# Kernel tuning notes

Hardware: AMD Instinct MI355X
Metric: run time of the kernel (lower is better)

The kernel has to match this reference:

```python
import jax, jax.numpy as jnp
import numpy as np


def setup_inputs() -> dict:
    key = jax.random.key(0)
    ks = jax.random.split(key, 9)
    B, C, H, W = 16, 512, 56, 56
    I = C // 2
    return {
        "x": jax.random.normal(ks[0], (B, C, H, W), dtype=jnp.float32),
        "g_w": jax.random.normal(ks[1], (I, C), dtype=jnp.float32) * 0.02,
        "g_b": jax.random.normal(ks[2], (I,), dtype=jnp.float32) * 0.02,
        "theta_w": jax.random.normal(ks[3], (I, C), dtype=jnp.float32) * 0.02,
        "theta_b": jax.random.normal(ks[4], (I,), dtype=jnp.float32) * 0.02,
        "phi_w": jax.random.normal(ks[5], (I, C), dtype=jnp.float32) * 0.02,
        "phi_b": jax.random.normal(ks[6], (I,), dtype=jnp.float32) * 0.02,
        "W_w": jax.random.normal(ks[7], (C, I), dtype=jnp.float32) * 0.02,
        "W_b": jax.random.normal(ks[8], (C,), dtype=jnp.float32) * 0.02,
    }


def reference(x, g_w, g_b, theta_w, theta_b, phi_w, phi_b, W_w, W_b):
    B, C, H, W = x.shape
    N = H * W
    xf = x.reshape(B, C, N)  # flatten spatial -> [B, C, N]
    # 1x1 convs == per-pixel channel matmuls
    g = jnp.einsum('ic,bcn->bin', g_w, xf) + g_b[:, None]        # [B, I, N]
    th = jnp.einsum('ic,bcn->bin', theta_w, xf) + theta_b[:, None]
    ph = jnp.einsum('ic,bcn->bin', phi_w, xf) + phi_b[:, None]
    # Original: y = (theta^T @ phi / N) @ g^T. No softmax -> reassociate:
    # y = theta^T @ ((phi @ g^T) / N), avoiding the [B, N, N] score matrix.
    M = jnp.einsum('bjn,bin->bji', ph, g) / N                    # [B, I, I]
    y = jnp.einsum('bjn,bji->bin', th, M)                        # [B, I, N]
    out = jnp.einsum('ci,bin->bcn', W_w, y) + W_b[:, None]       # [B, C, N]
    return x + out.reshape(B, C, H, W)
```

## Files before the change

kernel.cpp:

```cpp
#include <hip/hip_runtime.h>
#include <stdint.h>


typedef unsigned short ushort_t;
typedef __attribute__((ext_vector_type(8))) short short8;
typedef __attribute__((ext_vector_type(4))) float f32x4;
typedef __attribute__((ext_vector_type(8))) unsigned short us8;

#define NSP  3136

#define AS1(p) ((const __attribute__((address_space(1))) void*)(p))
#define AS3(p) ((__attribute__((address_space(3))) void*)(p))

__device__ inline ushort_t f2b(float f) {
  union { float f; uint32_t u; } c; c.f = f;
  uint32_t u = c.u;
  uint32_t r = (u + 0x7fffu + ((u >> 16) & 1u)) >> 16;
  return (ushort_t)r;
}

template<int MODE>
__global__ __launch_bounds__(256, 2) void gemm64(
    const ushort_t* __restrict__ Abase,
    const ushort_t* __restrict__ Bbase,
    void* __restrict__ Cbase, void* __restrict__ C2,
    const float* __restrict__ bias,
    const float* __restrict__ xres)
{
  constexpr int TB = 256;
  constexpr int CH = TB / 8;

  const int nwg = gridDim.x * gridDim.y * gridDim.z;
  int flat = blockIdx.x + gridDim.x * (blockIdx.y + gridDim.y * blockIdx.z);
  const int q = nwg >> 3;
  int swz = (flat & 7) * q + (flat >> 3);
  const int bx = swz % gridDim.x; int tmp = swz / gridDim.x;
  const int by = tmp % gridDim.y;
  const int bz = tmp / gridDim.y;

  int b = bz, kc = 0, kbeg = 0, kend, lda, ldb;
  const ushort_t *A, *B;
  if constexpr (MODE == 1) {
    A = Abase;
    B = Bbase + (size_t)b * 1605632;
    lda = 512; ldb = 512; kend = 512;
  } else if constexpr (MODE == 2) {
    b = bz & 15; kc = bz >> 4;
    A = Abase + (size_t)b * 1605632 + 802816;
    B = Abase + (size_t)b * 1605632;
    lda = NSP; ldb = NSP; kbeg = kc * 448; kend = kbeg + 448;
  } else if constexpr (MODE == 6) {
    A = Abase; lda = 256;
    B = Bbase + (size_t)b * 65536; ldb = 256;
    kend = 256;
  } else {
    A = Abase + (size_t)b * 131072; lda = 256;
    B = Bbase + (size_t)b * 819200; ldb = 256;
    kend = 256;
  }

  const int m0 = bx * 128;
  const int n0 = by * 128;
  const int tid = threadIdx.x;
  const int lane = tid & 63;
  const int wid = tid >> 6;
  const int wm = wid >> 1, wn = wid & 1;
  const int fr = lane & 15;
  const int fk = lane >> 4;

  __shared__ __align__(16) ushort_t SMu[32768];
  ushort_t (*As)[8192] = (ushort_t(*)[8192])(SMu);
  ushort_t (*Bs)[8192] = (ushort_t(*)[8192])(SMu + 16384);

  f32x4 acc[4][4];
#pragma unroll
  for (int i = 0; i < 4; ++i)
#pragma unroll
    for (int j = 0; j < 4; ++j) acc[i][j] = f32x4{0.f, 0.f, 0.f, 0.f};

  const int srow = tid >> 3;
  const int lsl = (tid & 7) ^ (srow & 7);
  const ushort_t* pa = A + (size_t)(m0 + srow) * lda + kbeg + lsl * 8;
  const ushort_t* pb = B + (size_t)(n0 + srow) * ldb + kbeg + lsl * 8;

#define STAGE(bufi) do {                                                              \
    __builtin_amdgcn_global_load_lds(AS1(pa),                    AS3(&As[bufi][tid * 8]), 16, 0, 0); \
    __builtin_amdgcn_global_load_lds(AS1(pa + (size_t)CH * lda), AS3(&As[bufi][TB * 8 + tid * 8]), 16, 0, 0); \
    __builtin_amdgcn_global_load_lds(AS1(pa + (size_t)2 * CH * lda), AS3(&As[bufi][2 * TB * 8 + tid * 8]), 16, 0, 0); \
    __builtin_amdgcn_global_load_lds(AS1(pa + (size_t)3 * CH * lda), AS3(&As[bufi][3 * TB * 8 + tid * 8]), 16, 0, 0); \
    __builtin_amdgcn_global_load_lds(AS1(pb),                    AS3(&Bs[bufi][tid * 8]), 16, 0, 0); \
    __builtin_amdgcn_global_load_lds(AS1(pb + (size_t)CH * ldb), AS3(&Bs[bufi][TB * 8 + tid * 8]), 16, 0, 0); \
    __builtin_amdgcn_global_load_lds(AS1(pb + (size_t)2 * CH * ldb), AS3(&Bs[bufi][2 * TB * 8 + tid * 8]), 16, 0, 0); \
    __builtin_amdgcn_global_load_lds(AS1(pb + (size_t)3 * CH * ldb), AS3(&Bs[bufi][3 * TB * 8 + tid * 8]), 16, 0, 0); \
    pa += 64; pb += 64;                                                               \
  } while (0)

  const int sw = fr & 7;
  const int s0 = ((0 | fk) ^ sw) * 8;
  const int s1 = ((4 | fk) ^ sw) * 8;
  const int arow = (wm * 64 + fr) * 64;
  const int brow = (wn * 64 + fr) * 64;

  asm volatile("s_waitcnt vmcnt(0)" ::: "memory");
  STAGE(0);

  const int nkt = (kend - kbeg) >> 6;
  for (int t = 0; t < nkt; ++t) {
    const int cur = t & 1;
    if (t + 1 < nkt) {
      STAGE(cur ^ 1);
      asm volatile("s_waitcnt vmcnt(8)" ::: "memory");
    } else {
      asm volatile("s_waitcnt vmcnt(0)" ::: "memory");
    }
    __builtin_amdgcn_s_barrier();
    __builtin_amdgcn_sched_barrier(0);

    short8 bf[4][2];
#pragma unroll
    for (int n = 0; n < 4; ++n) {
      bf[n][0] = *reinterpret_cast<const short8*>(&Bs[cur][brow + n * 1024 + s0]);
      bf[n][1] = *reinterpret_cast<const short8*>(&Bs[cur][brow + n * 1024 + s1]);
    }
    short8 af[4][2];
#pragma unroll
    for (int m = 0; m < 4; ++m) {
      af[m][0] = *reinterpret_cast<const short8*>(&As[cur][arow + m * 1024 + s0]);
      af[m][1] = *reinterpret_cast<const short8*>(&As[cur][arow + m * 1024 + s1]);
    }
    __builtin_amdgcn_s_setprio(1);
#pragma unroll
    for (int m = 0; m < 4; ++m)
#pragma unroll
      for (int n = 0; n < 4; ++n) {
        acc[m][n] = __builtin_amdgcn_mfma_f32_16x16x32_bf16(af[m][0], bf[n][0], acc[m][n], 0, 0, 0);
        acc[m][n] = __builtin_amdgcn_mfma_f32_16x16x32_bf16(af[m][1], bf[n][1], acc[m][n], 0, 0, 0);
      }
    __builtin_amdgcn_s_setprio(0);
    __builtin_amdgcn_s_barrier();
  }
#undef STAGE

  if constexpr (MODE == 1) {
    ushort_t* SMe = SMu;
    if (m0 < 512) {
#pragma unroll
      for (int m = 0; m < 4; ++m)
#pragma unroll
        for (int n = 0; n < 4; ++n) {
          int col = wn * 64 + n * 16 + fr;
#pragma unroll
          for (int r = 0; r < 4; ++r) {
            int row = wm * 64 + m * 16 + fk * 4 + r;
            SMe[row * 132 + col] = f2b(acc[m][n][r] + bias[m0 + row]);
          }
        }
      __builtin_amdgcn_s_barrier();
      ushort_t* P = (ushort_t*)Cbase;
#pragma unroll
      for (int it = 0; it < 8; ++it) {
        int idx = it * 256 + tid;
        int row = idx >> 4, ch = idx & 15;
        int gcol = n0 + ch * 8;
        if (gcol < NSP)
          *reinterpret_cast<us8*>(
              &P[(size_t)b * 512 * NSP + (size_t)(m0 + row) * NSP + gcol]) =
              *reinterpret_cast<const us8*>(&SMe[row * 132 + ch * 8]);
      }
    } else {
      const int j0 = m0 - 512;
#pragma unroll
      for (int m = 0; m < 4; ++m)
#pragma unroll
        for (int n = 0; n < 4; ++n) {
          int nl = wn * 64 + n * 16 + fr;
#pragma unroll
          for (int r = 0; r < 4; ++r) {
            int jl = wm * 64 + m * 16 + fk * 4 + r;
            SMe[nl * 132 + jl] = f2b(acc[m][n][r] + bias[512 + j0 + jl]);
          }
        }
      __builtin_amdgcn_s_barrier();
      ushort_t* thT = (ushort_t*)C2;
#pragma unroll
      for (int it = 0; it < 8; ++it) {
        int idx = it * 256 + tid;
        int row = idx >> 4, ch = idx & 15;
        int gn = n0 + row;
        if (gn < NSP)
          *reinterpret_cast<us8*>(
              &thT[(size_t)b * 819200 + (size_t)gn * 256 + j0 + ch * 8]) =
              *reinterpret_cast<const us8*>(&SMe[row * 132 + ch * 8]);
      }
    }
  } else if constexpr (MODE == 2) {
    float* Mf = (float*)Cbase;
#pragma unroll
    for (int m = 0; m < 4; ++m)
#pragma unroll
      for (int n = 0; n < 4; ++n) {
        int gcol = n0 + wn * 64 + n * 16 + fr;
#pragma unroll
        for (int r = 0; r < 4; ++r) {
          int grow = m0 + wm * 64 + m * 16 + fk * 4 + r;
          Mf[((size_t)kc * 16 + b) * 65536 + grow * 256 + gcol] = acc[m][n][r];
        }
      }
  } else if constexpr (MODE == 6) {
    ushort_t* U = (ushort_t*)Cbase;
#pragma unroll
    for (int m = 0; m < 4; ++m)
#pragma unroll
      for (int n = 0; n < 4; ++n) {
        int gcol = n0 + wn * 64 + n * 16 + fr;
#pragma unroll
        for (int r = 0; r < 4; ++r) {
          int grow = m0 + wm * 64 + m * 16 + fk * 4 + r;
          U[(size_t)b * 131072 + grow * 256 + gcol] = f2b(acc[m][n][r]);
        }
      }
  } else {
    float* out = (float*)Cbase;
    float* SMf = (float*)SMu;
#pragma unroll
    for (int p = 0; p < 2; ++p) {
      if (wm == p) {
#pragma unroll
        for (int m = 0; m < 4; ++m)
#pragma unroll
          for (int n = 0; n < 4; ++n) {
            int col = wn * 64 + n * 16 + fr;
#pragma unroll
            for (int r = 0; r < 4; ++r)
              SMf[(m * 16 + fk * 4 + r) * 132 + col] = acc[m][n][r];
          }
      }
      __builtin_amdgcn_s_barrier();
#pragma unroll
      for (int it = 0; it < 8; ++it) {
        int idx = it * 256 + tid;
        int row = idx >> 5, ch = idx & 31;
        int gcol = n0 + ch * 4;
        if (gcol < NSP) {
          int grow = m0 + p * 64 + row;
          size_t o = ((size_t)b * 512 + grow) * NSP + gcol;
          f32x4 v = *reinterpret_cast<const f32x4*>(&SMf[row * 132 + ch * 4]);
          f32x4 xr = *reinterpret_cast<const f32x4*>(&xres[o]);
          float bi = bias[grow];
          f32x4 ov = {v[0] + bi + xr[0], v[1] + bi + xr[1],
                      v[2] + bi + xr[2], v[3] + bi + xr[3]};
          *reinterpret_cast<f32x4*>(&out[o]) = ov;
        }
      }
      __builtin_amdgcn_s_barrier();
    }
  }
}

__global__ __launch_bounds__(256) void transp_x(const float* __restrict__ x,
                                                ushort_t* __restrict__ xb)
{
  const int nt = blockIdx.x, ct = blockIdx.y, b = blockIdx.z;
  const int t = threadIdx.x;
  const int n0 = nt * 64, c0 = ct * 64;
  __shared__ float Ls[64 * 65];

  const float* xs = x + (size_t)b * 512 * NSP;
#pragma unroll
  for (int p = 0; p < 4; ++p) {
    int cl = p * 16 + (t >> 4);
    int nl = (t & 15) * 4;
    f32x4 v = *reinterpret_cast<const f32x4*>(&xs[(size_t)(c0 + cl) * NSP + n0 + nl]);
    Ls[cl * 65 + nl + 0] = v[0];
    Ls[cl * 65 + nl + 1] = v[1];
    Ls[cl * 65 + nl + 2] = v[2];
    Ls[cl * 65 + nl + 3] = v[3];
  }
  __syncthreads();
#pragma unroll
  for (int it = 0; it < 2; ++it) {
    int idx = it * 256 + t; int nl = idx >> 3, cc = idx & 7;
    us8 o;
#pragma unroll
    for (int j = 0; j < 8; ++j) o[j] = f2b(Ls[(cc * 8 + j) * 65 + nl]);
    *reinterpret_cast<us8*>(&xb[((size_t)b * NSP + n0 + nl) * 512 + c0 + cc * 8]) = o;
  }
}

__global__ __launch_bounds__(256) void prep_weights(
    const float* __restrict__ g_w, const float* __restrict__ ph_w,
    const float* __restrict__ th_w, const float* __restrict__ W_w,
    const float* __restrict__ g_b, const float* __restrict__ ph_b,
    const float* __restrict__ th_b,
    ushort_t* __restrict__ W3, ushort_t* __restrict__ Wwb,
    float* __restrict__ bias3)
{
  int i = blockIdx.x * 256 + threadIdx.x;
  if (i < 393216) {
    int row = i >> 9, col = i & 511;
    float v = (row < 256) ? g_w[row * 512 + col]
            : (row < 512) ? ph_w[(row - 256) * 512 + col]
                          : th_w[(row - 512) * 512 + col];
    W3[i] = f2b(v);
  } else if (i < 524288) {
    Wwb[i - 393216] = f2b(W_w[i - 393216]);
  } else if (i < 525056) {
    int r = i - 524288;
    bias3[r] = (r < 256) ? g_b[r] : (r < 512) ? ph_b[r - 256] : th_b[r - 512];
  }
}

__global__ __launch_bounds__(256) void cvt_M(const float* __restrict__ Mf,
                                             ushort_t* __restrict__ MT)
{
  int i = blockIdx.x * 256 + threadIdx.x;
  const int SL = 1048576;
  float s = 0.f;
#pragma unroll
  for (int k = 0; k < 7; ++k) s += Mf[(size_t)k * SL + i];
  MT[i] = f2b(s * (1.0f / 3136.0f));
}

extern "C" void kernel_launch(void* const* d_in, const int* in_sizes, int n_in,
                              void* d_out, int out_size, void* d_ws, size_t ws_size,
                              hipStream_t stream) {
  const float* x    = (const float*)d_in[0];
  const float* g_w  = (const float*)d_in[1];
  const float* g_b  = (const float*)d_in[2];
  const float* th_w = (const float*)d_in[3];
  const float* th_b = (const float*)d_in[4];
  const float* ph_w = (const float*)d_in[5];
  const float* ph_b = (const float*)d_in[6];
  const float* W_w  = (const float*)d_in[7];
  const float* W_b  = (const float*)d_in[8];

  char* ws = (char*)d_ws;
  ushort_t* xb   = (ushort_t*)(ws + 0);
  float*    Mf2  = (float*)(ws + 0);
  ushort_t* MT2  = (ushort_t*)(ws + 29360128);
  ushort_t* U    = (ushort_t*)(ws + 31457280);
  ushort_t* P    = (ushort_t*)(ws + 51380224);
  ushort_t* thT  = (ushort_t*)(ws + 102760448);
  ushort_t* W3   = (ushort_t*)(ws + 128974848);
  ushort_t* Wwb  = (ushort_t*)(ws + 129761280);
  float*    bias3 = (float*)(ws + 130023424);

  prep_weights<<<2052, 256, 0, stream>>>(g_w, ph_w, th_w, W_w, g_b, ph_b, th_b,
                                         W3, Wwb, bias3);
  transp_x<<<dim3(49, 8, 16), 256, 0, stream>>>(x, xb);

  gemm64<1><<<dim3(6, 26, 16), 256, 0, stream>>>(W3, xb, P, thT, bias3, nullptr);
  gemm64<2><<<dim3(2, 2, 112), 256, 0, stream>>>(P, nullptr, Mf2, nullptr, nullptr, nullptr);
  cvt_M<<<4096, 256, 0, stream>>>(Mf2, MT2);
  gemm64<6><<<dim3(4, 2, 16), 256, 0, stream>>>(Wwb, MT2, U, nullptr, nullptr, nullptr);
  gemm64<4><<<dim3(4, 26, 16), 256, 0, stream>>>(U, thT, d_out, nullptr, W_b, x);
}
```

Baseline: 161.9 us.

## Store g/phi projections in FP8 and compute phi·gT with FP8 MFMA

The first GEMM now writes the g and phi projections as FP8 e4m3 bytes instead of bf16. A new dedicated kernel computes the I×I reduction over N with fp8 MFMA, using a byte-swizzled LDS layout. This halves the bytes written and re-read for the projection intermediate and doubles MFMA throughput for that stage. The cost is precision: e4m3 quantization of activations before a 3136-long reduction may raise error beyond tolerance.

After: 185.6 us. 1.15x slower.

```diff
diff --git a/kernel.cpp b/kernel.cpp
--- a/kernel.cpp
+++ b/kernel.cpp
@@ -17,6 +17,22 @@
   uint32_t u = c.u;
   uint32_t r = (u + 0x7fffu + ((u >> 16) & 1u)) >> 16;
   return (ushort_t)r;
+}
+
+__device__ inline unsigned char f2e4m3(float f) {
+  union { float f; uint32_t u; } c; c.f = f;
+  uint32_t s = (c.u >> 24) & 0x80;
+  float af = fabsf(f);
+  if (!(af >= 0x1p-6f)) return (unsigned char)s;
+  if (af > 448.f) af = 448.f;
+  c.f = af;
+  uint32_t u = c.u;
+  uint32_t md = (u >> 20) & 7;
+  uint32_t rem = u & 0xFFFFF;
+  uint32_t ee = ((u >> 23) & 0xFF) - 120;
+  if (rem > 0x80000u || (rem == 0x80000u && (md & 1))) { md++; if (md == 8) { md = 0; ee++; } }
+  if (ee > 15 || (ee == 15 && md > 6)) { ee = 15; md = 6; }
+  return (unsigned char)(s | (ee << 3) | md);
 }
 
 template<int MODE>
@@ -38,17 +54,12 @@
   const int by = tmp % gridDim.y;
   const int bz = tmp / gridDim.y;
 
-  int b = bz, kc = 0, kbeg = 0, kend, lda, ldb;
+  int b = bz, kend, lda, ldb;
   const ushort_t *A, *B;
   if constexpr (MODE == 1) {
     A = Abase;
     B = Bbase + (size_t)b * 1605632;
     lda = 512; ldb = 512; kend = 512;
-  } else if constexpr (MODE == 2) {
-    b = bz & 15; kc = bz >> 4;
-    A = Abase + (size_t)b * 1605632 + 802816;
-    B = Abase + (size_t)b * 1605632;
-    lda = NSP; ldb = NSP; kbeg = kc * 448; kend = kbeg + 448;
   } else if constexpr (MODE == 6) {
     A = Abase; lda = 256;
     B = Bbase + (size_t)b * 65536; ldb = 256;
@@ -80,8 +91,8 @@
 
   const int srow = tid >> 3;
   const int lsl = (tid & 7) ^ (srow & 7);
-  const ushort_t* pa = A + (size_t)(m0 + srow) * lda + kbeg + lsl * 8;
-  const ushort_t* pb = B + (size_t)(n0 + srow) * ldb + kbeg + lsl * 8;
+  const ushort_t* pa = A + (size_t)(m0 + srow) * lda + lsl * 8;
+  const ushort_t* pb = B + (size_t)(n0 + srow) * ldb + lsl * 8;
 
 #define STAGE(bufi) do {                                                              \
     __builtin_amdgcn_global_load_lds(AS1(pa),                    AS3(&As[bufi][tid * 8]), 16, 0, 0); \
@@ -104,7 +115,7 @@
   asm volatile("s_waitcnt vmcnt(0)" ::: "memory");
   STAGE(0);
 
-  const int nkt = (kend - kbeg) >> 6;
+  const int nkt = kend >> 6;
   for (int t = 0; t < nkt; ++t) {
     const int cur = t & 1;
     if (t + 1 < nkt) {
@@ -142,8 +153,8 @@
 #undef STAGE
 
   if constexpr (MODE == 1) {
-    ushort_t* SMe = SMu;
     if (m0 < 512) {
+      unsigned char* SMe8 = (unsigned char*)SMu;
 #pragma unroll
       for (int m = 0; m < 4; ++m)
 #pragma unroll
@@ -152,22 +163,23 @@
 #pragma unroll
           for (int r = 0; r < 4; ++r) {
             int row = wm * 64 + m * 16 + fk * 4 + r;
-            SMe[row * 132 + col] = f2b(acc[m][n][r] + bias[m0 + row]);
+            SMe8[row * 144 + col] = f2e4m3(acc[m][n][r] + bias[m0 + row]);
           }
         }
       __builtin_amdgcn_s_barrier();
-      ushort_t* P = (ushort_t*)Cbase;
-#pragma unroll
-      for (int it = 0; it < 8; ++it) {
+      unsigned char* P8 = (unsigned char*)Cbase;
+#pragma unroll
+      for (int it = 0; it < 4; ++it) {
         int idx = it * 256 + tid;
-        int row = idx >> 4, ch = idx & 15;
-        int gcol = n0 + ch * 8;
+        int row = idx >> 3, ch = idx & 7;
+        int gcol = n0 + ch * 16;
         if (gcol < NSP)
-          *reinterpret_cast<us8*>(
-              &P[(size_t)b * 512 * NSP + (size_t)(m0 + row) * NSP + gcol]) =
-              *reinterpret_cast<const us8*>(&SMe[row * 132 + ch * 8]);
+          *reinterpret_cast<uint4*>(
+              &P8[(size_t)b * 1605632 + (size_t)(m0 + row) * NSP + gcol]) =
+              *reinterpret_cast<const uint4*>(&SMe8[row * 144 + ch * 16]);
       }
     } else {
+      ushort_t* SMe = SMu;
       const int j0 = m0 - 512;
 #pragma unroll
       for (int m = 0; m < 4; ++m)
@@ -193,19 +205,6 @@
               *reinterpret_cast<const us8*>(&SMe[row * 132 + ch * 8]);
       }
     }
-  } else if constexpr (MODE == 2) {
-    float* Mf = (float*)Cbase;
-#pragma unroll
-    for (int m = 0; m < 4; ++m)
-#pragma unroll
-      for (int n = 0; n < 4; ++n) {
-        int gcol = n0 + wn * 64 + n * 16 + fr;
-#pragma unroll
-        for (int r = 0; r < 4; ++r) {
-          int grow = m0 + wm * 64 + m * 16 + fk * 4 + r;
-          Mf[((size_t)kc * 16 + b) * 65536 + grow * 256 + gcol] = acc[m][n][r];
-        }
-      }
   } else if constexpr (MODE == 6) {
     ushort_t* U = (ushort_t*)Cbase;
 #pragma unroll
@@ -255,6 +254,110 @@
       __builtin_amdgcn_s_barrier();
     }
   }
+}
+
+__global__ __launch_bounds__(256, 2) void g2_fp8(
+    const unsigned char* __restrict__ P8, float* __restrict__ Mf)
+{
+  const int nwg = gridDim.x * gridDim.y * gridDim.z;
+  int flat = blockIdx.x + gridDim.x * (blockIdx.y + gridDim.y * blockIdx.z);
+  const int q = nwg >> 3;
+  int swz = (flat & 7) * q + (flat >> 3);
+  const int bx = swz % gridDim.x; int tmp = swz / gridDim.x;
+  const int by = tmp % gridDim.y;
+  const int bz = tmp / gridDim.y;
+  const int b = bz & 15, kc = bz >> 4;
+
+  const unsigned char* A = P8 + (size_t)b * 1605632 + 802816;
+  const unsigned char* B = P8 + (size_t)b * 1605632;
+  const int kbeg = kc * 448;
+
+  const int m0 = bx * 128, n0 = by * 128;
+  const int tid = threadIdx.x;
+  const int lane = tid & 63;
+  const int wid = tid >> 6;
+  const int wm = wid >> 1, wn = wid & 1;
+  const int fr = lane & 15;
+  const int fk = lane >> 4;
+
+  __shared__ __align__(16) unsigned char As8[2][8192];
+  __shared__ __align__(16) unsigned char Bs8[2][8192];
+
+  f32x4 acc[4][4];
+#pragma unroll
+  for (int i = 0; i < 4; ++i)
+#pragma unroll
+    for (int j = 0; j < 4; ++j) acc[i][j] = f32x4{0.f, 0.f, 0.f, 0.f};
+
+  const int swzs = ((tid >> 2) & 3) ^ ((tid >> 4) & 3);
+  const unsigned char* pa = A + (size_t)((tid >> 2)) * NSP + kbeg + ((tid & 3) ^ swzs) * 16;
+  const unsigned char* pb = B + (size_t)((tid >> 2)) * NSP + kbeg + ((tid & 3) ^ swzs) * 16;
+  pa += (size_t)m0 * NSP;
+  pb += (size_t)n0 * NSP;
+
+#define STAGE8(bufi) do { \
+    __builtin_amdgcn_global_load_lds(AS1(pa), AS3(&As8[bufi][tid * 16]), 16, 0, 0); \
+    __builtin_amdgcn_global_load_lds(AS1(pa + (size_t)64 * NSP), AS3(&As8[bufi][4096 + tid * 16]), 16, 0, 0); \
+    __builtin_amdgcn_global_load_lds(AS1(pb), AS3(&Bs8[bufi][tid * 16]), 16, 0, 0); \
+    __builtin_amdgcn_global_load_lds(AS1(pb + (size_t)64 * NSP), AS3(&Bs8[bufi][4096 + tid * 16]), 16, 0, 0); \
+    pa += 64; pb += 64; \
+  } while (0)
+
+  const int swzr = (fr & 3) ^ ((fr >> 2) & 3);
+  const int fo0 = (((fk >> 1) + 0) ^ swzr) * 16 + (fk & 1) * 8;
+  const int fo1 = (((fk >> 1) + 2) ^ swzr) * 16 + (fk & 1) * 8;
+  const int arow = (wm * 64 + fr) * 64;
+  const int brow = (wn * 64 + fr) * 64;
+
+  asm volatile("s_waitcnt vmcnt(0)" ::: "memory");
+  STAGE8(0);
+
+  for (int t = 0; t < 7; ++t) {
+    const int cur = t & 1;
+    if (t + 1 < 7) {
+      STAGE8(cur ^ 1);
+      asm volatile("s_waitcnt vmcnt(4)" ::: "memory");
+    } else {
+      asm volatile("s_waitcnt vmcnt(0)" ::: "memory");
+    }
+    __builtin_amdgcn_s_barrier();
+    __builtin_amdgcn_sched_barrier(0);
+
+    long a8[4][2], b8[4][2];
+#pragma unroll
+    for (int n = 0; n < 4; ++n) {
+      b8[n][0] = *reinterpret_cast<const long*>(&Bs8[cur][brow + n * 1024 + fo0]);
+      b8[n][1] = *reinterpret_cast<const long*>(&Bs8[cur][brow + n * 1024 + fo1]);
+    }
+#pragma unroll
+    for (int m = 0; m < 4; ++m) {
+      a8[m][0] = *reinterpret_cast<const long*>(&As8[cur][arow + m * 1024 + fo0]);
+      a8[m][1] = *reinterpret_cast<const long*>(&As8[cur][arow + m * 1024 + fo1]);
+    }
+    __builtin_amdgcn_s_setprio(1);
+#pragma unroll
+    for (int m = 0; m < 4; ++m)
+#pragma unroll
+      for (int n = 0; n < 4; ++n) {
+        acc[m][n] = __builtin_amdgcn_mfma_f32_16x16x32_fp8_fp8(a8[m][0], b8[n][0], acc[m][n], 0, 0, 0);
+        acc[m][n] = __builtin_amdgcn_mfma_f32_16x16x32_fp8_fp8(a8[m][1], b8[n][1], acc[m][n], 0, 0, 0);
+      }
+    __builtin_amdgcn_s_setprio(0);
+    __builtin_amdgcn_s_barrier();
+  }
+#undef STAGE8
+
+#pragma unroll
+  for (int m = 0; m < 4; ++m)
+#pragma unroll
+    for (int n = 0; n < 4; ++n) {
+      int gcol = n0 + wn * 64 + n * 16 + fr;
+#pragma unroll
+      for (int r = 0; r < 4; ++r) {
+        int grow = m0 + wm * 64 + m * 16 + fk * 4 + r;
+        Mf[((size_t)kc * 16 + b) * 65536 + grow * 256 + gcol] = acc[m][n][r];
+      }
+    }
 }
 
 __global__ __launch_bounds__(256) void transp_x(const float* __restrict__ x,
@@ -335,22 +438,22 @@
   const float* W_b  = (const float*)d_in[8];
 
   char* ws = (char*)d_ws;
-  ushort_t* xb   = (ushort_t*)(ws + 0);
-  float*    Mf2  = (float*)(ws + 0);
-  ushort_t* MT2  = (ushort_t*)(ws + 29360128);
-  ushort_t* U    = (ushort_t*)(ws + 31457280);
-  ushort_t* P    = (ushort_t*)(ws + 51380224);
-  ushort_t* thT  = (ushort_t*)(ws + 102760448);
-  ushort_t* W3   = (ushort_t*)(ws + 128974848);
-  ushort_t* Wwb  = (ushort_t*)(ws + 129761280);
-  float*    bias3 = (float*)(ws + 130023424);
+  ushort_t*      xb   = (ushort_t*)(ws + 0);
+  float*         Mf2  = (float*)(ws + 0);
+  ushort_t*      MT2  = (ushort_t*)(ws + 29360128);
+  ushort_t*      U    = (ushort_t*)(ws + 31457280);
+  unsigned char* P8   = (unsigned char*)(ws + 51380224);
+  ushort_t*      thT  = (ushort_t*)(ws + 77070336);
+  ushort_t*      W3   = (ushort_t*)(ws + 103415808);
+  ushort_t*      Wwb  = (ushort_t*)(ws + 104202240);
+  float*         bias3 = (float*)(ws + 104464384);
 
   prep_weights<<<2052, 256, 0, stream>>>(g_w, ph_w, th_w, W_w, g_b, ph_b, th_b,
                                          W3, Wwb, bias3);
   transp_x<<<dim3(49, 8, 16), 256, 0, stream>>>(x, xb);
 
-  gemm64<1><<<dim3(6, 26, 16), 256, 0, stream>>>(W3, xb, P, thT, bias3, nullptr);
-  gemm64<2><<<dim3(2, 2, 112), 256, 0, stream>>>(P, nullptr, Mf2, nullptr, nullptr, nullptr);
+  gemm64<1><<<dim3(6, 26, 16), 256, 0, stream>>>(W3, xb, P8, thT, bias3, nullptr);
+  g2_fp8<<<dim3(2, 2, 112), 256, 0, stream>>>(P8, Mf2);
   cvt_M<<<4096, 256, 0, stream>>>(Mf2, MT2);
   gemm64<6><<<dim3(4, 2, 16), 256, 0, stream>>>(Wwb, MT2, U, nullptr, nullptr, nullptr);
   gemm64<4><<<dim3(4, 26, 16), 256, 0, stream>>>(U, thT, d_out, nullptr, W_b, x);
```
